# Kernel optimization log

Measured on AMD Instinct MI355X. Metric: run time of the kernel, lower is better.

Reference implementation:

```python
import jax, jax.numpy as jnp
import numpy as np

H = 16       # num_heads
DH = 64      # dim_head
SCALE = DH ** -0.5


def setup_inputs() -> dict:
    key = jax.random.key(0)
    k1, k2 = jax.random.split(key)
    ZT = jax.random.normal(k1, (2, 2048, 1024), dtype=jnp.float32)
    # Linear weight, shape (H*dh, dim); scaled like a typical init for stability
    W = jax.random.normal(k2, (1024, 1024), dtype=jnp.float32) * 0.02
    return {"ZT": ZT, "W": W}


def reference(ZT, W):
    b, n, dim = ZT.shape
    # UT(ZT): ZT @ W^T -> (b, n, H*dh), reshape to (b, h, n, dh)
    ZTU = jnp.einsum('bnd,ed->bne', ZT, W).reshape(b, n, H, DH).transpose(0, 2, 1, 3)
    # scores = ZTU @ ZTU^T * scale  (b, h, n, n)
    scores = jnp.einsum('bhnd,bhmd->bhnm', ZTU, ZTU) * SCALE
    attn = jax.nn.softmax(scores, axis=-1)  # dropout p=0 -> identity
    # attn @ ZTU -> (b, h, n, dh) -> (b, n, H*dh)
    ssa = jnp.einsum('bhnm,bhmd->bhnd', attn, ZTU)
    ssa = ssa.transpose(0, 2, 1, 3).reshape(b, n, H * DH)
    # UT(I).T == W (shape (H*dh, dim)); final projection back to dim
    mssa = jnp.einsum('bne,ed->bnd', ssa, W)
    # return_proj=False path: module returns (MSSA_out, MSSA_out)
    return (mssa, mssa)
```

## Files before the change

### kernel.cpp

```cpp
#include <hip/hip_runtime.h>
#include <hip/hip_bf16.h>
#include <stdint.h>

typedef __attribute__((ext_vector_type(8))) short bf16x8;
typedef __attribute__((ext_vector_type(4))) float f32x4;

#define MFMA16(a, b, c) __builtin_amdgcn_mfma_f32_16x16x32_bf16(a, b, c, 0, 0, 0)

typedef const __attribute__((address_space(1))) unsigned int* as1_u32p;
typedef __attribute__((address_space(3))) unsigned int* as3_u32p;
__device__ __forceinline__ void gl_lds16(const void* g, void* l) {
    __builtin_amdgcn_global_load_lds((as1_u32p)g, (as3_u32p)l, 16, 0, 0);
}

__device__ __forceinline__ unsigned short f2bs(float f) {
    __hip_bfloat16 h = __float2bfloat16(f);
    unsigned short s;
    __builtin_memcpy(&s, &h, 2);
    return s;
}

__device__ __forceinline__ unsigned int pk_bf16(float a, float b) {
    float2 f; f.x = a; f.y = b;
    __hip_bfloat162 h = __float22bfloat162_rn(f);
    unsigned int u;
    __builtin_memcpy(&u, &h, 4);
    return u;
}

__device__ __forceinline__ float exp2_fast(float x) {
    return __builtin_amdgcn_exp2f(x);
}

#define QSCALE 0.18033688f

__global__ __launch_bounds__(256) void cvt_k(const float* __restrict__ w,
                                             const float* __restrict__ zt,
                                             unsigned short* __restrict__ wbf,
                                             unsigned short* __restrict__ wtbf,
                                             unsigned short* __restrict__ ztbf) {
    __shared__ __attribute__((aligned(16))) unsigned short T[64 * 72];
    const int tid = threadIdx.x;
    if (blockIdx.x >= 256) {
        const int i = ((int)blockIdx.x - 256) * 2048 + tid * 8;
        const float4 v0 = *(const float4*)(zt + i);
        const float4 v1 = *(const float4*)(zt + i + 4);
        uint4 wv;
        wv.x = pk_bf16(v0.x, v0.y);
        wv.y = pk_bf16(v0.z, v0.w);
        wv.z = pk_bf16(v1.x, v1.y);
        wv.w = pk_bf16(v1.z, v1.w);
        *(uint4*)(ztbf + i) = wv;
        return;
    }
    const int b2 = blockIdx.x;
    const int e0 = (b2 >> 4) * 64, d0 = (b2 & 15) * 64;
    const int el = tid >> 2;
    const int dl = (tid & 3) * 16;
    const float* src = w + (size_t)(e0 + el) * 1024 + d0 + dl;
    unsigned short myv[16];
#pragma unroll
    for (int q = 0; q < 4; ++q) {
        const float4 v = *(const float4*)(src + q * 4);
        myv[q * 4 + 0] = f2bs(v.x);
        myv[q * 4 + 1] = f2bs(v.y);
        myv[q * 4 + 2] = f2bs(v.z);
        myv[q * 4 + 3] = f2bs(v.w);
    }
    *(bf16x8*)(wbf + (size_t)(e0 + el) * 1024 + d0 + dl) = *(const bf16x8*)&myv[0];
    *(bf16x8*)(wbf + (size_t)(e0 + el) * 1024 + d0 + dl + 8) = *(const bf16x8*)&myv[8];
#pragma unroll
    for (int q = 0; q < 16; ++q) T[(dl + q) * 72 + el] = myv[q];
    __syncthreads();
#pragma unroll
    for (int p = 0; p < 2; ++p) {
        const int idx = p * 256 + tid;
        const int dd = idx >> 3, c = (idx & 7) * 8;
        const bf16x8 v = *(const bf16x8*)&T[dd * 72 + c];
        *(bf16x8*)(wtbf + (size_t)(d0 + dd) * 1024 + e0 + c) = v;
    }
}

template <int EPI>
__global__ __launch_bounds__(256, 2) void gemm_bt_k(
    const __hip_bfloat16* __restrict__ Abf, const __hip_bfloat16* __restrict__ B,
    unsigned short* __restrict__ ztu, unsigned short* __restrict__ ztut,
    float* __restrict__ out0, float* __restrict__ out1) {
    __shared__ __attribute__((aligned(16))) unsigned short smem[24576];
    unsigned short* Tb = smem;

    const int p = blockIdx.x;
    const int bm = (p & 7) * 8 + ((p >> 3) & 7);
    const int bn = p >> 6;
    const int tid = threadIdx.x;
    const int wave = tid >> 6, lane = tid & 63;
    const int wm = wave >> 1, wn = wave & 1;
    const int quad = lane >> 4, l16 = lane & 15;

    f32x4 acc[2][4] = {};

    const int lrow = lane >> 3;
    const int sw = (lane & 7) ^ lrow;
    const __hip_bfloat16* Ag0 = Abf + (size_t)(bm * 64 + (2 * wave) * 8 + lrow) * 1024 + sw * 8;
    const __hip_bfloat16* Ag1 = Ag0 + 8 * 1024;
    const __hip_bfloat16* Bg0 = B + (size_t)(bn * 128 + (4 * wave) * 8 + lrow) * 1024 + sw * 8;
    const __hip_bfloat16* Bg1 = Bg0 + 8 * 1024;
    const __hip_bfloat16* Bg2 = Bg0 + 16 * 1024;
    const __hip_bfloat16* Bg3 = Bg0 + 24 * 1024;

    auto stage = [&](int ko, unsigned short* sb) {
        gl_lds16(Ag0 + ko, sb + (2 * wave) * 512);
        gl_lds16(Ag1 + ko, sb + (2 * wave + 1) * 512);
        gl_lds16(Bg0 + ko, sb + 4096 + (4 * wave) * 512);
        gl_lds16(Bg1 + ko, sb + 4096 + (4 * wave + 1) * 512);
        gl_lds16(Bg2 + ko, sb + 4096 + (4 * wave + 2) * 512);
        gl_lds16(Bg3 + ko, sb + 4096 + (4 * wave + 3) * 512);
    };

    const int ch0 = (quad ^ (l16 & 7)) * 8;
    const int ch1 = ch0 ^ 32;
    const int raA = (wm * 32 + l16) * 64;
    const int raB = (wn * 64 + l16) * 64;

    stage(0, smem);
    __syncthreads();

    for (int kt = 0; kt < 16; ++kt) {
        unsigned short* const sb = smem + (kt & 1) * 12288;
        if (kt < 15) stage((kt + 1) << 6, smem + (((kt & 1) ^ 1) * 12288));
        bf16x8 af[2][2], bfr[2][4];
#pragma unroll
        for (int i = 0; i < 2; ++i) {
            af[0][i] = *(const bf16x8*)&sb[raA + i * 1024 + ch0];
            af[1][i] = *(const bf16x8*)&sb[raA + i * 1024 + ch1];
        }
#pragma unroll
        for (int j = 0; j < 4; ++j) {
            bfr[0][j] = *(const bf16x8*)&sb[4096 + raB + j * 1024 + ch0];
            bfr[1][j] = *(const bf16x8*)&sb[4096 + raB + j * 1024 + ch1];
        }
#pragma unroll
        for (int h = 0; h < 2; ++h)
#pragma unroll
            for (int i = 0; i < 2; ++i)
#pragma unroll
                for (int j = 0; j < 4; ++j) acc[i][j] = MFMA16(af[h][i], bfr[h][j], acc[i][j]);
        __syncthreads();
    }

    if (EPI == 0) {
        const int h = bn * 2 + wn;
        const int bb = bm >> 5;
        const int nb = (bm & 31) * 64;
        const size_t hb = (size_t)(bb * 16 + h) * 131072;
#pragma unroll
        for (int i = 0; i < 2; ++i) {
#pragma unroll
            for (int r = 0; r < 4; ++r) {
                const int n = nb + wm * 32 + i * 16 + quad * 4 + r;
                uint2 pk;
                pk.x = pk_bf16(acc[i][0][r], acc[i][1][r]);
                pk.y = pk_bf16(acc[i][2][r], acc[i][3][r]);
                *(uint2*)(ztu + hb + n * 64 + l16 * 4) = pk;
                const int npl = wm * 32 + quad * 8 + i * 4 + r;
                Tb[(wn * 64 + 0 + l16) * 72 + npl] = (unsigned short)(pk.x & 0xffff);
                Tb[(wn * 64 + 16 + l16) * 72 + npl] = (unsigned short)(pk.x >> 16);
                Tb[(wn * 64 + 32 + l16) * 72 + npl] = (unsigned short)(pk.y & 0xffff);
                Tb[(wn * 64 + 48 + l16) * 72 + npl] = (unsigned short)(pk.y >> 16);
            }
        }
        __syncthreads();
#pragma unroll
        for (int ee = 0; ee < 4; ++ee) {
            const int e_local = wave * 32 + ee * 8 + (lane >> 3);
            const int nc = (lane & 7) * 8;
            const bf16x8 v = *(const bf16x8*)&Tb[e_local * 72 + nc];
            const int hh = bn * 2 + (e_local >> 6);
            const int dh = e_local & 63;
            *(bf16x8*)(ztut + (size_t)(bb * 16 + hh) * 131072 + dh * 2048 + nb + nc) = v;
        }
    } else {
        float* Tf = (float*)smem;
#pragma unroll
        for (int i = 0; i < 2; ++i)
#pragma unroll
            for (int r = 0; r < 4; ++r) {
                const int ml = wm * 32 + i * 16 + quad * 4 + r;
#pragma unroll
                for (int j = 0; j < 4; ++j)
                    Tf[ml * 132 + wn * 64 + j * 16 + l16] = acc[i][j][r];
            }
        __syncthreads();
#pragma unroll
        for (int q = 0; q < 8; ++q) {
            const int idx = q * 256 + tid;
            const int row = idx >> 5;
            const int c4 = (idx & 31) * 4;
            const float4 v = *(const float4*)&Tf[row * 132 + c4];
            const size_t off = (size_t)(bm * 64 + row) * 1024 + bn * 128 + c4;
            *(float4*)(out0 + off) = v;
            *(float4*)(out1 + off) = v;
        }
    }
}

__global__ __launch_bounds__(256, 2) void attn_k(const unsigned short* __restrict__ ztu,
                                                 const unsigned short* __restrict__ ztut,
                                                 unsigned short* __restrict__ ssa) {
    __shared__ __attribute__((aligned(16))) unsigned short Kt[2][4096];
    __shared__ __attribute__((aligned(16))) unsigned short Vt[2][4096];
    const int p = blockIdx.x;
    const int ii = p >> 3;
    const int bh = (p & 7) * 4 + (ii >> 5);
    const int qt = ii & 31;
    const int tid = threadIdx.x, wave = tid >> 6, lane = tid & 63;
    const int quad = lane >> 4, l16 = lane & 15;
    const unsigned short* base = ztu + (size_t)bh * 131072;
    const unsigned short* baseT = ztut + (size_t)bh * 131072;

    const int qrow = qt * 64 + wave * 16;
    bf16x8 qa[2];
    qa[0] = *(const bf16x8*)(base + (qrow + l16) * 64 + quad * 8);
    qa[1] = *(const bf16x8*)(base + (qrow + l16) * 64 + 32 + quad * 8);
#pragma unroll
    for (int w = 0; w < 2; ++w) {
        bf16x8 v = qa[w], r;
#pragma unroll
        for (int z = 0; z < 8; z += 2) {
            const float f0 = __uint_as_float(((unsigned)(unsigned short)v[z]) << 16) * QSCALE;
            const float f1 = __uint_as_float(((unsigned)(unsigned short)v[z + 1]) << 16) * QSCALE;
            const unsigned u = pk_bf16(f0, f1);
            r[z] = (short)(u & 0xffff);
            r[z + 1] = (short)(u >> 16);
        }
        qa[w] = r;
    }

    f32x4 o[4] = {};
    f32x4 lacc = {};
    bf16x8 ones;
#pragma unroll
    for (int z = 0; z < 8; ++z) ones[z] = (short)0x3f80;

    const int c0 = wave * 2, c1 = c0 + 1;
    const int lrow = lane >> 3;
    const int sw = (lane & 7) ^ lrow;
    const unsigned short* gK0 = base + (c0 * 8 + lrow) * 64 + sw * 8;
    const unsigned short* gK1 = base + (c1 * 8 + lrow) * 64 + sw * 8;
    const unsigned short* gV0 = baseT + (size_t)(c0 * 8 + lrow) * 2048 + sw * 8;
    const unsigned short* gV1 = baseT + (size_t)(c1 * 8 + lrow) * 2048 + sw * 8;

    const int swq = (quad ^ (l16 & 7));
    const int koff0 = l16 * 64 + swq * 8;
    const int koff1 = l16 * 64 + (swq ^ 4) * 8;

    for (int tp = 0; tp < 16; ++tp) {
        const int t0 = tp * 2;
        gl_lds16(gK0 + t0 * 4096, &Kt[0][c0 * 512]);
        gl_lds16(gK1 + t0 * 4096, &Kt[0][c1 * 512]);
        gl_lds16(gV0 + t0 * 64, &Vt[0][c0 * 512]);
        gl_lds16(gV1 + t0 * 64, &Vt[0][c1 * 512]);
        gl_lds16(gK0 + t0 * 4096 + 4096, &Kt[1][c0 * 512]);
        gl_lds16(gK1 + t0 * 4096 + 4096, &Kt[1][c1 * 512]);
        gl_lds16(gV0 + t0 * 64 + 64, &Vt[1][c0 * 512]);
        gl_lds16(gV1 + t0 * 64 + 64, &Vt[1][c1 * 512]);
        __syncthreads();

#pragma unroll
        for (int u = 0; u < 2; ++u) {
            f32x4 st[4];
#pragma unroll
            for (int nf = 0; nf < 4; ++nf) {
                const bf16x8 kb0 = *(const bf16x8*)&Kt[u][nf * 1024 + koff0];
                const bf16x8 kb1 = *(const bf16x8*)&Kt[u][nf * 1024 + koff1];
                f32x4 z = {0.f, 0.f, 0.f, 0.f};
                z = MFMA16(kb0, qa[0], z);
                z = MFMA16(kb1, qa[1], z);
                st[nf] = z;
            }

            float e[16];
#pragma unroll
            for (int nf = 0; nf < 4; ++nf)
#pragma unroll
                for (int r = 0; r < 4; ++r) e[nf * 4 + r] = exp2_fast(st[nf][r]);
            bf16x8 pa[2];
            uint4 u0, u1;
            u0.x = pk_bf16(e[0], e[1]);   u0.y = pk_bf16(e[2], e[3]);
            u0.z = pk_bf16(e[4], e[5]);   u0.w = pk_bf16(e[6], e[7]);
            u1.x = pk_bf16(e[8], e[9]);   u1.y = pk_bf16(e[10], e[11]);
            u1.z = pk_bf16(e[12], e[13]); u1.w = pk_bf16(e[14], e[15]);
            __builtin_memcpy(&pa[0], &u0, 16);
            __builtin_memcpy(&pa[1], &u1, 16);
            lacc = MFMA16(ones, pa[0], lacc);
            lacc = MFMA16(ones, pa[1], lacc);

#pragma unroll
            for (int df = 0; df < 4; ++df) {
                const bf16x8 vb0 = *(const bf16x8*)&Vt[u][df * 1024 + koff0];
                const bf16x8 vb1 = *(const bf16x8*)&Vt[u][df * 1024 + koff1];
                o[df] = MFMA16(vb0, pa[0], o[df]);
                o[df] = MFMA16(vb1, pa[1], o[df]);
            }
        }
        __syncthreads();
    }

    const int b = bh >> 4, h = bh & 15;
    const float inv = 1.0f / lacc[0];
    const int token = b * 2048 + qrow + l16;
#pragma unroll
    for (int df = 0; df < 4; ++df) {
        uint2 pk;
        pk.x = pk_bf16(o[df][0] * inv, o[df][1] * inv);
        pk.y = pk_bf16(o[df][2] * inv, o[df][3] * inv);
        *(uint2*)(ssa + (size_t)token * 1024 + h * 64 + df * 16 + quad * 4) = pk;
    }
}

extern "C" void kernel_launch(void* const* d_in, const int* in_sizes, int n_in,
                              void* d_out, int out_size, void* d_ws, size_t ws_size,
                              hipStream_t stream) {
    const float* ZT = (const float*)d_in[0];
    const float* W = (const float*)d_in[1];
    float* out = (float*)d_out;
    char* ws = (char*)d_ws;

    unsigned short* wbf   = (unsigned short*)(ws);
    unsigned short* wtbf  = (unsigned short*)(ws + 2u * 1024 * 1024);
    unsigned short* ztu   = (unsigned short*)(ws + 4u * 1024 * 1024);
    unsigned short* ztut  = (unsigned short*)(ws + 12u * 1024 * 1024);
    unsigned short* scr20 = (unsigned short*)(ws + 20u * 1024 * 1024);

    cvt_k<<<2304, 256, 0, stream>>>(W, ZT, wbf, wtbf, scr20);
    gemm_bt_k<0><<<512, 256, 0, stream>>>((const __hip_bfloat16*)scr20,
                                          (const __hip_bfloat16*)wbf, ztu, ztut,
                                          nullptr, nullptr);
    attn_k<<<1024, 256, 0, stream>>>(ztu, ztut, scr20);
    gemm_bt_k<1><<<512, 256, 0, stream>>>((const __hip_bfloat16*)scr20,
                                          (const __hip_bfloat16*)wtbf, nullptr, nullptr,
                                          out, out + 4194304);
}
```

Before: 147.0 us.

## Process two 16-row query groups per wave in attention kernel

Each wave now handles 32 query rows (two 16-row groups) instead of 16, so each workgroup covers 128 queries and the grid halves to 512 blocks. Every K and V fragment loaded from LDS and every global-to-LDS tile load is reused across twice as many queries. This cuts LDS traffic and global reloads of K/V per unit of work. In exchange, register pressure roughly doubles for accumulators and there are fewer blocks to fill the CUs, which may reduce occupancy or latency hiding.

```diff
diff --git a/kernel.cpp b/kernel.cpp
--- a/kernel.cpp
+++ b/kernel.cpp
@@ -211,33 +211,36 @@
     __shared__ __attribute__((aligned(16))) unsigned short Vt[2][4096];
     const int p = blockIdx.x;
     const int ii = p >> 3;
-    const int bh = (p & 7) * 4 + (ii >> 5);
-    const int qt = ii & 31;
+    const int bh = (p & 7) * 4 + (ii >> 4);
+    const int qt = ii & 15;
     const int tid = threadIdx.x, wave = tid >> 6, lane = tid & 63;
     const int quad = lane >> 4, l16 = lane & 15;
     const unsigned short* base = ztu + (size_t)bh * 131072;
     const unsigned short* baseT = ztut + (size_t)bh * 131072;
 
-    const int qrow = qt * 64 + wave * 16;
-    bf16x8 qa[2];
-    qa[0] = *(const bf16x8*)(base + (qrow + l16) * 64 + quad * 8);
-    qa[1] = *(const bf16x8*)(base + (qrow + l16) * 64 + 32 + quad * 8);
-#pragma unroll
-    for (int w = 0; w < 2; ++w) {
-        bf16x8 v = qa[w], r;
-#pragma unroll
-        for (int z = 0; z < 8; z += 2) {
-            const float f0 = __uint_as_float(((unsigned)(unsigned short)v[z]) << 16) * QSCALE;
-            const float f1 = __uint_as_float(((unsigned)(unsigned short)v[z + 1]) << 16) * QSCALE;
-            const unsigned u = pk_bf16(f0, f1);
-            r[z] = (short)(u & 0xffff);
-            r[z + 1] = (short)(u >> 16);
-        }
-        qa[w] = r;
-    }
-
-    f32x4 o[4] = {};
-    f32x4 lacc = {};
+    const int qb = qt * 128 + wave * 32;
+    bf16x8 qa[2][2];
+#pragma unroll
+    for (int g = 0; g < 2; ++g) {
+        qa[g][0] = *(const bf16x8*)(base + (qb + g * 16 + l16) * 64 + quad * 8);
+        qa[g][1] = *(const bf16x8*)(base + (qb + g * 16 + l16) * 64 + 32 + quad * 8);
+#pragma unroll
+        for (int w = 0; w < 2; ++w) {
+            bf16x8 v = qa[g][w], r;
+#pragma unroll
+            for (int z = 0; z < 8; z += 2) {
+                const float f0 = __uint_as_float(((unsigned)(unsigned short)v[z]) << 16) * QSCALE;
+                const float f1 = __uint_as_float(((unsigned)(unsigned short)v[z + 1]) << 16) * QSCALE;
+                const unsigned u = pk_bf16(f0, f1);
+                r[z] = (short)(u & 0xffff);
+                r[z + 1] = (short)(u >> 16);
+            }
+            qa[g][w] = r;
+        }
+    }
+
+    f32x4 o[2][4] = {};
+    f32x4 lacc[2] = {};
     bf16x8 ones;
 #pragma unroll
     for (int z = 0; z < 8; ++z) ones[z] = (short)0x3f80;
@@ -268,53 +271,65 @@
 
 #pragma unroll
         for (int u = 0; u < 2; ++u) {
-            f32x4 st[4];
+            f32x4 st[2][4];
 #pragma unroll
             for (int nf = 0; nf < 4; ++nf) {
                 const bf16x8 kb0 = *(const bf16x8*)&Kt[u][nf * 1024 + koff0];
                 const bf16x8 kb1 = *(const bf16x8*)&Kt[u][nf * 1024 + koff1];
-                f32x4 z = {0.f, 0.f, 0.f, 0.f};
-                z = MFMA16(kb0, qa[0], z);
-                z = MFMA16(kb1, qa[1], z);
-                st[nf] = z;
-            }
-
-            float e[16];
-#pragma unroll
-            for (int nf = 0; nf < 4; ++nf)
-#pragma unroll
-                for (int r = 0; r < 4; ++r) e[nf * 4 + r] = exp2_fast(st[nf][r]);
-            bf16x8 pa[2];
-            uint4 u0, u1;
-            u0.x = pk_bf16(e[0], e[1]);   u0.y = pk_bf16(e[2], e[3]);
-            u0.z = pk_bf16(e[4], e[5]);   u0.w = pk_bf16(e[6], e[7]);
-            u1.x = pk_bf16(e[8], e[9]);   u1.y = pk_bf16(e[10], e[11]);
-            u1.z = pk_bf16(e[12], e[13]); u1.w = pk_bf16(e[14], e[15]);
-            __builtin_memcpy(&pa[0], &u0, 16);
-            __builtin_memcpy(&pa[1], &u1, 16);
-            lacc = MFMA16(ones, pa[0], lacc);
-            lacc = MFMA16(ones, pa[1], lacc);
+#pragma unroll
+                for (int g = 0; g < 2; ++g) {
+                    f32x4 z = {0.f, 0.f, 0.f, 0.f};
+                    z = MFMA16(kb0, qa[g][0], z);
+                    z = MFMA16(kb1, qa[g][1], z);
+                    st[g][nf] = z;
+                }
+            }
+
+            bf16x8 pa[2][2];
+#pragma unroll
+            for (int g = 0; g < 2; ++g) {
+                float e[16];
+#pragma unroll
+                for (int nf = 0; nf < 4; ++nf)
+#pragma unroll
+                    for (int r = 0; r < 4; ++r) e[nf * 4 + r] = exp2_fast(st[g][nf][r]);
+                uint4 u0, u1;
+                u0.x = pk_bf16(e[0], e[1]);   u0.y = pk_bf16(e[2], e[3]);
+                u0.z = pk_bf16(e[4], e[5]);   u0.w = pk_bf16(e[6], e[7]);
+                u1.x = pk_bf16(e[8], e[9]);   u1.y = pk_bf16(e[10], e[11]);
+                u1.z = pk_bf16(e[12], e[13]); u1.w = pk_bf16(e[14], e[15]);
+                __builtin_memcpy(&pa[g][0], &u0, 16);
+                __builtin_memcpy(&pa[g][1], &u1, 16);
+                lacc[g] = MFMA16(ones, pa[g][0], lacc[g]);
+                lacc[g] = MFMA16(ones, pa[g][1], lacc[g]);
+            }
 
 #pragma unroll
             for (int df = 0; df < 4; ++df) {
                 const bf16x8 vb0 = *(const bf16x8*)&Vt[u][df * 1024 + koff0];
                 const bf16x8 vb1 = *(const bf16x8*)&Vt[u][df * 1024 + koff1];
-                o[df] = MFMA16(vb0, pa[0], o[df]);
-                o[df] = MFMA16(vb1, pa[1], o[df]);
+#pragma unroll
+                for (int g = 0; g < 2; ++g) {
+                    o[g][df] = MFMA16(vb0, pa[g][0], o[g][df]);
+                    o[g][df] = MFMA16(vb1, pa[g][1], o[g][df]);
+                }
             }
         }
         __syncthreads();
     }
 
     const int b = bh >> 4, h = bh & 15;
-    const float inv = 1.0f / lacc[0];
-    const int token = b * 2048 + qrow + l16;
-#pragma unroll
-    for (int df = 0; df < 4; ++df) {
-        uint2 pk;
-        pk.x = pk_bf16(o[df][0] * inv, o[df][1] * inv);
-        pk.y = pk_bf16(o[df][2] * inv, o[df][3] * inv);
-        *(uint2*)(ssa + (size_t)token * 1024 + h * 64 + df * 16 + quad * 4) = pk;
+#pragma unroll
+    for (int g = 0; g < 2; ++g) {
+        const float inv = 1.0f / lacc[g][0];
+        const int token = b * 2048 + qb + g * 16 + l16;
+#pragma unroll
+        for (int df = 0; df < 4; ++df) {
+            uint2 pk;
+            pk.x = pk_bf16(o[g][df][0] * inv, o[g][df][1] * inv);
+            pk.y = pk_bf16(o[g][df][2] * inv, o[g][df][3] * inv);
+            *(uint2*)(ssa + (size_t)token * 1024 + h * 64 + df * 16 + quad * 4) = pk;
+        }
     }
 }
 
@@ -336,7 +351,7 @@
     gemm_bt_k<0><<<512, 256, 0, stream>>>((const __hip_bfloat16*)scr20,
                                           (const __hip_bfloat16*)wbf, ztu, ztut,
                                           nullptr, nullptr);
-    attn_k<<<1024, 256, 0, stream>>>(ztu, ztut, scr20);
+    attn_k<<<512, 256, 0, stream>>>(ztu, ztut, scr20);
     gemm_bt_k<1><<<512, 256, 0, stream>>>((const __hip_bfloat16*)scr20,
                                           (const __hip_bfloat16*)wtbf, nullptr, nullptr,
                                           out, out + 4194304);
```

Result: faster. 143.6 us (-2.3%).
